# Performance work log

Measured on AMD Instinct MI355X. Metric: run time of the kernel, lower is better.

The kernel has to match this reference:

```python
import jax, jax.numpy as jnp
import numpy as np

BZ, N, NH, HD = 256, 360, 4, 8  # batch, roi_num, num_heads, head_dim
POOL_L = int(N * 0.7)  # 252


def _lrelu(x):
    return jax.nn.leaky_relu(x, 0.2)


def _bn(x, g, b):
    # training-mode BatchNorm1d over flattened (bz*roi) dim, biased variance, eps=1e-5
    mu = x.mean(0)
    var = x.var(0)
    return (x - mu) * jax.lax.rsqrt(var + 1e-5) * g + b


def setup_inputs() -> dict:
    key = jax.random.key(0)
    ks = jax.random.split(key, 20)
    def rn(i, shape, s=0.05):
        return jax.random.normal(ks[i], shape, dtype=jnp.float32) * s
    z = lambda *s: jnp.zeros(s, jnp.float32)
    o = lambda *s: jnp.ones(s, jnp.float32)
    return {
        "m": jax.random.normal(ks[0], (BZ, N, N), dtype=jnp.float32),
        "node_feature": jax.random.normal(ks[1], (BZ, N, N), dtype=jnp.float32),
        "cls": rn(2, (1, 16)),
        "gcn0_w": rn(3, (N, N)), "gcn0_b": z(N),
        "gcn1_w": rn(4, (N, N)), "gcn1_b": z(N),
        "gcn2_w1": rn(5, (N, 64)), "gcn2_b1": z(64),
        "gcn2_w2": rn(6, (64, 16)), "gcn2_b2": z(16),
        "sc_w": rn(7, (N, 16)), "sc_b": z(16),
        "bn0_g": o(N), "bn0_b": z(N),
        "bn1_g": o(N), "bn1_b": z(N),
        "bn2_g": o(16), "bn2_b": z(16),
        "wq": rn(8, (16, NH * HD)), "bq": z(NH * HD),
        "wk": rn(9, (16, NH * HD)), "bk": z(NH * HD),
        "wv": rn(10, (16, NH * HD)), "bv": z(NH * HD),
        "wo": rn(11, (NH * HD, 16)), "bo": z(16),
        "f1_w": rn(12, (16, 64)), "f1_b": z(64),
        "f2_w": rn(13, (64, 32)), "f2_b": z(32),
        "f3_w": rn(14, (32, 2)), "f3_b": z(2),
    }


def reference(m, node_feature, cls, gcn0_w, gcn0_b, gcn1_w, gcn1_b,
              gcn2_w1, gcn2_b1, gcn2_w2, gcn2_b2, sc_w, sc_b,
              bn0_g, bn0_b, bn1_g, bn1_b, bn2_g, bn2_b,
              wq, bq, wk, bk, wv, bv, wo, bo,
              f1_w, f1_b, f2_w, f2_b, f3_w, f3_b):
    bz, n = m.shape[0], m.shape[1]
    # einsum('ijk,ijp->ijp', m, x) == rowsum(m) * x (elementwise), faithful to source
    rowsum = m.sum(-1, keepdims=True)  # [bz, n, 1]

    x_clone = jnp.zeros_like(node_feature)
    x = node_feature
    # layer 0
    x = rowsum * x
    x = _lrelu(x @ gcn0_w + gcn0_b) + x_clone
    x = _bn(x.reshape(bz * n, -1), bn0_g, bn0_b).reshape(bz, n, -1)
    x_clone = x
    # layer 1
    x = rowsum * x
    x = _lrelu(x @ gcn1_w + gcn1_b) + x_clone
    x = _bn(x.reshape(bz * n, -1), bn1_g, bn1_b).reshape(bz, n, -1)
    x_clone = x
    # layer 2 (with shortcut projection)
    x = rowsum * x
    h = _lrelu(_lrelu(x @ gcn2_w1 + gcn2_b1) @ gcn2_w2 + gcn2_b2)
    x = h + _lrelu(x_clone @ sc_w + sc_b)
    x = _bn(x.reshape(bz * n, -1), bn2_g, bn2_b).reshape(bz, n, 16)

    # prepend cls token (vectorized, replaces the per-sample python loop)
    x_in = jnp.concatenate([jnp.broadcast_to(cls, (bz, 1, 16)), x], axis=1)  # [bz, n+1, 16]

    # Encoder: multi-head self-attention
    q = (x_in @ wq + bq).reshape(bz, n + 1, NH, HD)
    k = (x_in @ wk + bk).reshape(bz, n + 1, NH, HD)
    v = (x_in @ wv + bv).reshape(bz, n + 1, NH, HD)
    scale = 1.0 / jnp.sqrt(jnp.asarray(HD, jnp.float32))
    attn = jax.nn.softmax(jnp.einsum('bqhd,bkhd->bhqk', q, k) * scale, axis=-1)  # [bz,4,n+1,n+1]
    out = jnp.einsum('bhqk,bkhd->bqhd', attn, v).reshape(bz, n + 1, NH * HD) @ wo + bo  # [bz,n+1,16]

    # cls-row attention summed over 4 heads, drop cls column
    score = attn[:, :, 0, :].sum(1)[:, 1:]  # [bz, n]
    sc = score
    vals, idx = jax.lax.top_k(score, POOL_L)  # top-l sort/gather
    w = jax.nn.softmax(vals, axis=-1)  # [bz, l]
    x_body = out[:, 1:, :]  # [bz, n, 16]
    x_p = jnp.take_along_axis(x_body, idx[:, :, None], axis=1)  # [bz, l, 16]
    pooled = jnp.einsum('bl,bld->bd', w, x_p)  # [bz, 16]

    h = _lrelu(pooled @ f1_w + f1_b)
    h = _lrelu(h @ f2_w + f2_b)
    logits = h @ f3_w + f3_b  # [bz, 2]
    return (logits, jax.nn.sigmoid(sc), attn)
```

## Files before the change

kernel.cpp:

```cpp
#include <hip/hip_runtime.h>
#include <math.h>

#define BZ 256
#define NN 360
#define NP1 361
#define MROWS (BZ*NN)
#define POOLL 252
#define KP 384

typedef __attribute__((ext_vector_type(8))) short bf16x8;
typedef __attribute__((ext_vector_type(4))) float f32x4;

__device__ __forceinline__ float lrelu(float x){ return x > 0.f ? x : 0.2f*x; }

__device__ __forceinline__ ushort f2bf(float f){
    union { float f; uint u; } v; v.f = f;
    uint u = v.u + 0x7FFFu + ((v.u >> 16) & 1u);
    return (ushort)(u >> 16);
}
__device__ __forceinline__ float bf2f(ushort h){
    union { uint u; float f; } v; v.u = ((uint)h) << 16;
    return v.f;
}
__device__ __forceinline__ void split2(float v, ushort& hi, ushort& lo){
    hi = f2bf(v);
    lo = f2bf(v - bf2f(hi));
}

__device__ __forceinline__ void gload16(const void* g, void* l){
    __builtin_amdgcn_global_load_lds((const __attribute__((address_space(1))) uint*)g,
                                     (__attribute__((address_space(3))) uint*)l, 16, 0, 0);
}

__device__ __forceinline__ void stage_plane(const ushort* __restrict__ src, size_t srow0,
                                            ushort (*P)[32], int k0, int t){
    int w = t >> 6;
    #pragma unroll
    for (int i=0;i<2;i++){
        int u = i*256 + t;
        int row = u >> 2, ccs = u & 3;
        int cg = ccs ^ ((row >> 1) & 3);
        const ushort* g = src + (srow0 + row)*KP + k0 + cg*8;
        char* l = (char*)P + i*4096 + w*1024;
        gload16(g, l);
    }
}

__device__ __forceinline__ bf16x8 frag_read(const ushort (*P)[32], int row, int g){
    return *(const bf16x8*)((const char*)P + row*64 + ((g ^ ((row >> 1) & 3)) * 16));
}

__global__ void k_zero(float* p, int n){
    int i = blockIdx.x*blockDim.x + threadIdx.x;
    if (i < n) p[i] = 0.f;
}

__global__ __launch_bounds__(256)
void k_rowsum(const float* __restrict__ m, float* __restrict__ rowsum){
    int wid = (blockIdx.x*blockDim.x + threadIdx.x) >> 6;
    int lane = threadIdx.x & 63;
    if (wid >= MROWS) return;
    const float4* p = (const float4*)(m + (size_t)wid*NN);
    float s = 0.f;
    {
        float4 f = p[lane];
        s += f.x + f.y + f.z + f.w;
    }
    if (lane < 26){
        float4 f = p[64 + lane];
        s += f.x + f.y + f.z + f.w;
    }
    #pragma unroll
    for (int off = 32; off; off >>= 1) s += __shfl_down(s, off);
    if (lane == 0) rowsum[wid] = s;
}

__global__ __launch_bounds__(384)
void k_prepw(const float* __restrict__ W, int ncols, int joff,
             const float* __restrict__ s, const float* __restrict__ h,
             ushort* __restrict__ Wth, ushort* __restrict__ Wtl, float* __restrict__ cvec)
{
    int j = blockIdx.x;
    int k = threadIdx.x;
    __shared__ float red[6];
    float wv = 0.f, hv = 0.f, sv = 1.f;
    if (k < NN && j < ncols){
        wv = W[(size_t)k*ncols + j];
        if (s) sv = s[k];
        if (h) hv = h[k];
    }
    ushort hi, lo; split2(wv * sv, hi, lo);
    Wth[(size_t)(joff + j)*KP + k] = hi;
    Wtl[(size_t)(joff + j)*KP + k] = lo;
    float v = hv * wv;
    #pragma unroll
    for (int off = 32; off; off >>= 1) v += __shfl_down(v, off);
    int lane = k & 63, wid = k >> 6;
    if (lane == 0) red[wid] = v;
    __syncthreads();
    if (k == 0) cvec[joff + j] = red[0]+red[1]+red[2]+red[3]+red[4]+red[5];
}

template<bool AF32, bool RESID>
__global__ __launch_bounds__(256)
void k_gemm_mfma(const void* __restrict__ Avh, const ushort* __restrict__ Avl,
                 const ushort* __restrict__ Wth, const ushort* __restrict__ Wtl,
                 const float* __restrict__ cvec, const float* __restrict__ bias,
                 const float* __restrict__ rowsum,
                 const float* __restrict__ bns, const float* __restrict__ bnh,
                 ushort* __restrict__ Yhi, ushort* __restrict__ Ylo,
                 float* __restrict__ colsum, float* __restrict__ colsq)
{
    __shared__ ushort Ah[128][32];
    __shared__ ushort Al[128][32];
    __shared__ ushort Bh[128][32];
    __shared__ ushort Bl[128][32];
    int t = threadIdx.x;
    int w = t >> 6, lane = t & 63;
    int l15 = lane & 15, g = lane >> 4;
    int idx = blockIdx.x;
    int gr = idx & 7;
    int rem = idx >> 3;
    int jcb = rem % 3;
    int gq = rem / 3;
    int rowblk = (gq*8 + gr) * 128;
    int colblk = jcb * 128;

    f32x4 acc[2][8];
    #pragma unroll
    for (int i=0;i<2;i++)
        #pragma unroll
        for (int j=0;j<8;j++)
            #pragma unroll
            for (int e=0;e<4;e++) acc[i][j][e] = 0.f;

    for (int kt = 0; kt < 12; ++kt){
        int k0 = kt * 32;
        if (AF32){
            const float* A = (const float*)Avh;
            int row = t >> 1, half = t & 1;
            int fr = (row >> 1) & 3;
            #pragma unroll
            for (int c=0;c<2;c++){
                int cg = half*2 + c;
                int k = k0 + cg*8;
                float4 f0 = make_float4(0.f,0.f,0.f,0.f);
                float4 f1 = make_float4(0.f,0.f,0.f,0.f);
                if (k < NN){
                    f0 = *(const float4*)&A[(size_t)(rowblk+row)*NN + k];
                    f1 = *(const float4*)&A[(size_t)(rowblk+row)*NN + k + 4];
                }
                ushort h0,l0,h1,l1,h2,l2,h3,l3,h4,l4,h5,l5,h6,l6,h7,l7;
                split2(f0.x,h0,l0); split2(f0.y,h1,l1); split2(f0.z,h2,l2); split2(f0.w,h3,l3);
                split2(f1.x,h4,l4); split2(f1.y,h5,l5); split2(f1.z,h6,l6); split2(f1.w,h7,l7);
                uint4 hv = make_uint4((uint)h0|((uint)h1<<16), (uint)h2|((uint)h3<<16),
                                      (uint)h4|((uint)h5<<16), (uint)h6|((uint)h7<<16));
                uint4 lv = make_uint4((uint)l0|((uint)l1<<16), (uint)l2|((uint)l3<<16),
                                      (uint)l4|((uint)l5<<16), (uint)l6|((uint)l7<<16));
                int ccs = cg ^ fr;
                *(uint4*)((char*)Ah + row*64 + ccs*16) = hv;
                *(uint4*)((char*)Al + row*64 + ccs*16) = lv;
            }
        } else {
            stage_plane((const ushort*)Avh, (size_t)rowblk, Ah, k0, t);
            stage_plane(Avl,               (size_t)rowblk, Al, k0, t);
        }
        stage_plane(Wth, (size_t)colblk, Bh, k0, t);
        stage_plane(Wtl, (size_t)colblk, Bl, k0, t);
        __syncthreads();

        bf16x8 ah0 = frag_read(Ah, 32*w + l15, g);
        bf16x8 ah1 = frag_read(Ah, 32*w + 16 + l15, g);
        bf16x8 al0 = frag_read(Al, 32*w + l15, g);
        bf16x8 al1 = frag_read(Al, 32*w + 16 + l15, g);
        #pragma unroll
        for (int nj=0;nj<8;nj++){
            bf16x8 bh = frag_read(Bh, 16*nj + l15, g);
            bf16x8 bl = frag_read(Bl, 16*nj + l15, g);
            acc[0][nj] = __builtin_amdgcn_mfma_f32_16x16x32_bf16(ah0, bh, acc[0][nj], 0, 0, 0);
            acc[0][nj] = __builtin_amdgcn_mfma_f32_16x16x32_bf16(al0, bh, acc[0][nj], 0, 0, 0);
            acc[0][nj] = __builtin_amdgcn_mfma_f32_16x16x32_bf16(ah0, bl, acc[0][nj], 0, 0, 0);
            acc[1][nj] = __builtin_amdgcn_mfma_f32_16x16x32_bf16(ah1, bh, acc[1][nj], 0, 0, 0);
            acc[1][nj] = __builtin_amdgcn_mfma_f32_16x16x32_bf16(al1, bh, acc[1][nj], 0, 0, 0);
            acc[1][nj] = __builtin_amdgcn_mfma_f32_16x16x32_bf16(ah1, bl, acc[1][nj], 0, 0, 0);
        }
        __syncthreads();
    }

    const ushort* AHg = (const ushort*)Avh;
    float cs_part[8] = {0,0,0,0,0,0,0,0}, cq_part[8] = {0,0,0,0,0,0,0,0};
    #pragma unroll
    for (int mi=0;mi<2;mi++){
        #pragma unroll
        for (int nj=0;nj<8;nj++){
            f32x4 d = acc[mi][nj];
            #pragma unroll
            for (int r=0;r<4;r++){
                int row = rowblk + 32*w + 16*mi + 4*g + r;
                int col = colblk + 16*nj + l15;
                float v = 0.f;
                if (col < NN){
                    float pre = rowsum[row] * (d[r] + cvec[col]) + bias[col];
                    v = lrelu(pre);
                    if (RESID){
                        size_t ai = (size_t)row*KP + col;
                        float ar = bf2f(AHg[ai]) + bf2f(Avl[ai]);
                        v += ar * bns[col] + bnh[col];
                    }
                }
                ushort hi, lo; split2(v, hi, lo);
                Yhi[(size_t)row*KP + col] = hi;
                Ylo[(size_t)row*KP + col] = lo;
                cs_part[nj] += v;
                cq_part[nj] += v*v;
            }
        }
    }
    #pragma unroll
    for (int nj=0;nj<8;nj++){
        cs_part[nj] += __shfl_xor(cs_part[nj], 16); cs_part[nj] += __shfl_xor(cs_part[nj], 32);
        cq_part[nj] += __shfl_xor(cq_part[nj], 16); cq_part[nj] += __shfl_xor(cq_part[nj], 32);
    }
    float* red = (float*)&Ah[0][0];
    if (lane < 16){
        #pragma unroll
        for (int nj=0;nj<8;nj++) red[w*128 + nj*16 + l15] = cs_part[nj];
    }
    __syncthreads();
    if (t < 128 && colblk + t < NN)
        atomicAdd(&colsum[colblk + t], red[t] + red[128+t] + red[256+t] + red[384+t]);
    __syncthreads();
    if (lane < 16){
        #pragma unroll
        for (int nj=0;nj<8;nj++) red[w*128 + nj*16 + l15] = cq_part[nj];
    }
    __syncthreads();
    if (t < 128 && colblk + t < NN)
        atomicAdd(&colsq[colblk + t], red[t] + red[128+t] + red[256+t] + red[384+t]);
}

__global__ void k_bnfin(const float* __restrict__ colsum, const float* __restrict__ colsq,
                        const float* __restrict__ g, const float* __restrict__ b, int ncols,
                        float* __restrict__ scale, float* __restrict__ shift){
    int j = blockIdx.x*blockDim.x + threadIdx.x;
    if (j >= ncols) return;
    float mu = colsum[j] / (float)MROWS;
    float var = colsq[j] / (float)MROWS - mu*mu;
    float sc = g[j] * rsqrtf(var + 1e-5f);
    scale[j] = sc;
    shift[j] = b[j] - mu*sc;
}

__global__ __launch_bounds__(256)
void k_gemm2_mfma(const ushort* __restrict__ AH, const ushort* __restrict__ AL,
                  const ushort* __restrict__ Wth, const ushort* __restrict__ Wtl,
                  const float* __restrict__ cvec, const float* __restrict__ b1,
                  const float* __restrict__ scb, const float* __restrict__ rowsum,
                  float* __restrict__ h1buf, float* __restrict__ scbuf)
{
    __shared__ ushort Ah[128][32];
    __shared__ ushort Al[128][32];
    __shared__ ushort Bh[80][40];
    __shared__ ushort Bl[80][40];
    int t = threadIdx.x;
    int w = t >> 6, lane = t & 63;
    int l15 = lane & 15, g = lane >> 4;
    int rowblk = blockIdx.x * 128;

    f32x4 acc[2][5];
    #pragma unroll
    for (int i=0;i<2;i++)
        #pragma unroll
        for (int j=0;j<5;j++)
            #pragma unroll
            for (int e=0;e<4;e++) acc[i][j][e] = 0.f;

    for (int kt = 0; kt < 12; ++kt){
        int k0 = kt * 32;
        stage_plane(AH, (size_t)rowblk, Ah, k0, t);
        stage_plane(AL, (size_t)rowblk, Al, k0, t);
        #pragma unroll
        for (int l=0;l<2;l++){
            int c = t + l*256;
            if (c < 320){
                int col = c >> 2, kk = (c & 3)*8;
                ((int4*)&Bh[col][kk])[0] = *(const int4*)&Wth[(size_t)col*KP + k0 + kk];
                ((int4*)&Bl[col][kk])[0] = *(const int4*)&Wtl[(size_t)col*KP + k0 + kk];
            }
        }
        __syncthreads();
        bf16x8 ah0 = frag_read(Ah, 32*w + l15, g);
        bf16x8 ah1 = frag_read(Ah, 32*w + 16 + l15, g);
        bf16x8 al0 = frag_read(Al, 32*w + l15, g);
        bf16x8 al1 = frag_read(Al, 32*w + 16 + l15, g);
        #pragma unroll
        for (int nj=0;nj<5;nj++){
            bf16x8 bh = *(const bf16x8*)&Bh[16*nj + l15][8*g];
            bf16x8 bl = *(const bf16x8*)&Bl[16*nj + l15][8*g];
            acc[0][nj] = __builtin_amdgcn_mfma_f32_16x16x32_bf16(ah0, bh, acc[0][nj], 0, 0, 0);
            acc[0][nj] = __builtin_amdgcn_mfma_f32_16x16x32_bf16(al0, bh, acc[0][nj], 0, 0, 0);
            acc[0][nj] = __builtin_amdgcn_mfma_f32_16x16x32_bf16(ah0, bl, acc[0][nj], 0, 0, 0);
            acc[1][nj] = __builtin_amdgcn_mfma_f32_16x16x32_bf16(ah1, bh, acc[1][nj], 0, 0, 0);
            acc[1][nj] = __builtin_amdgcn_mfma_f32_16x16x32_bf16(al1, bh, acc[1][nj], 0, 0, 0);
            acc[1][nj] = __builtin_amdgcn_mfma_f32_16x16x32_bf16(ah1, bl, acc[1][nj], 0, 0, 0);
        }
        __syncthreads();
    }

    #pragma unroll
    for (int mi=0;mi<2;mi++){
        #pragma unroll
        for (int nj=0;nj<5;nj++){
            f32x4 d = acc[mi][nj];
            #pragma unroll
            for (int r=0;r<4;r++){
                int row = rowblk + 32*w + 16*mi + 4*g + r;
                int col = 16*nj + l15;
                if (nj < 4){
                    float pre = rowsum[row] * (d[r] + cvec[col]) + b1[col];
                    h1buf[(size_t)row*64 + col] = lrelu(pre);
                } else {
                    int cc = col - 64;
                    float pre = d[r] + cvec[col] + scb[cc];
                    scbuf[(size_t)row*16 + cc] = lrelu(pre);
                }
            }
        }
    }
}

__global__ __launch_bounds__(256)
void k_stage2(const float* __restrict__ h1buf, const float* __restrict__ scbuf,
              const float* __restrict__ w2, const float* __restrict__ b2,
              float* __restrict__ x2, float* __restrict__ colsum, float* __restrict__ colsq)
{
    __shared__ float Hs[64][65];
    __shared__ float Ws[64][17];
    __shared__ float red[16][16];
    int t = threadIdx.x;
    int rowblk = blockIdx.x * 64;
    #pragma unroll
    for (int l=0;l<4;l++){
        int idx = t + l*256;
        Ws[idx>>4][idx&15] = w2[idx];
    }
    #pragma unroll
    for (int l=0;l<16;l++){
        int idx = t + l*256;
        Hs[idx>>6][idx&63] = h1buf[(size_t)rowblk*64 + idx];
    }
    __syncthreads();
    int col = t & 15, rb = t >> 4;
    float ps=0.f, pq=0.f;
    #pragma unroll
    for (int gg=0; gg<4; gg++){
        int r = rb + gg*16;
        float s = b2[col];
        #pragma unroll
        for (int c=0;c<64;c++) s += Hs[r][c]*Ws[c][col];
        float v = lrelu(s) + scbuf[(size_t)(rowblk+r)*16 + col];
        x2[(size_t)(rowblk+r)*16 + col] = v;
        ps += v; pq += v*v;
    }
    red[rb][col] = ps; __syncthreads();
    if (t < 16){
        float s=0.f;
        for (int g=0; g<16; g++) s += red[g][t];
        atomicAdd(&colsum[t], s);
    }
    __syncthreads();
    red[rb][col] = pq; __syncthreads();
    if (t < 16){
        float s=0.f;
        for (int g=0; g<16; g++) s += red[g][t];
        atomicAdd(&colsq[t], s);
    }
}

__global__ __launch_bounds__(256)
void k_qkv(const float* __restrict__ x2, const float* __restrict__ s2, const float* __restrict__ h2,
           const float* __restrict__ cls,
           const float* __restrict__ wq, const float* __restrict__ bq,
           const float* __restrict__ wk, const float* __restrict__ bk,
           const float* __restrict__ wv, const float* __restrict__ bv,
           float* __restrict__ qkv)
{
    int b = blockIdx.x;
    __shared__ float4 xin[NP1][4];
    int t = threadIdx.x;
    for (int i = t; i < NP1*4; i += 256){
        int r = i >> 2, c4 = i & 3;
        float4 f;
        if (r == 0) f = ((const float4*)cls)[c4];
        else {
            f = *(const float4*)&x2[((size_t)b*NN + r-1)*16 + c4*4];
            f.x = f.x*s2[c4*4+0] + h2[c4*4+0];
            f.y = f.y*s2[c4*4+1] + h2[c4*4+1];
            f.z = f.z*s2[c4*4+2] + h2[c4*4+2];
            f.w = f.w*s2[c4*4+3] + h2[c4*4+3];
        }
        xin[r][c4] = f;
    }
    __syncthreads();
    for (int task = t; task < 3*NP1*8; task += 256){
        int tn = task / (NP1*8);
        int rem = task - tn*(NP1*8);
        int r = rem >> 3, d4 = rem & 7;
        const float* W  = (tn==0) ? wq : ((tn==1) ? wk : wv);
        const float* Bb = (tn==0) ? bq : ((tn==1) ? bk : bv);
        float o0 = Bb[d4*4+0], o1 = Bb[d4*4+1], o2 = Bb[d4*4+2], o3 = Bb[d4*4+3];
        #pragma unroll
        for (int c4=0;c4<4;c4++){
            float4 xf = xin[r][c4];
            float xs[4] = {xf.x, xf.y, xf.z, xf.w};
            #pragma unroll
            for (int cc=0;cc<4;cc++){
                int c = c4*4 + cc;
                float x = xs[cc];
                o0 += x * W[c*32 + d4*4 + 0];
                o1 += x * W[c*32 + d4*4 + 1];
                o2 += x * W[c*32 + d4*4 + 2];
                o3 += x * W[c*32 + d4*4 + 3];
            }
        }
        if (tn == 0){
            const float sc = 0.35355339059327373f;
            o0 *= sc; o1 *= sc; o2 *= sc; o3 *= sc;
        }
        *(float4*)&qkv[(((size_t)b*3 + tn)*NP1 + r)*32 + d4*4] = make_float4(o0,o1,o2,o3);
    }
}

__device__ __forceinline__ float bfly8(float o[8], int lane){
    int b0 = lane & 1, b1 = lane & 2, b2 = lane & 4;
    float n[4];
    #pragma unroll
    for (int j=0;j<4;j++){
        float give = b0 ? o[j] : o[j+4];
        float keep = b0 ? o[j+4] : o[j];
        n[j] = keep + __shfl_xor(give, 1);
    }
    float m2[2];
    #pragma unroll
    for (int j=0;j<2;j++){
        float give = b1 ? n[j] : n[j+2];
        float keep = b1 ? n[j+2] : n[j];
        m2[j] = keep + __shfl_xor(give, 2);
    }
    float give = b2 ? m2[0] : m2[1];
    float keep = b2 ? m2[1] : m2[0];
    float v = keep + __shfl_xor(give, 4);
    v += __shfl_xor(v, 8);
    v += __shfl_xor(v, 16);
    v += __shfl_xor(v, 32);
    return v;
}

__global__ __launch_bounds__(256)
void k_attn(const float* __restrict__ qkv, float* __restrict__ attn, float* __restrict__ obuf)
{
    int blk = blockIdx.x;
    int chunk = blk & 1;
    int bh = blk >> 1;
    int b = bh >> 2, h = bh & 3;
    __shared__ float4 KV[4][NP1];
    __shared__ float4 QS[2][NP1];
    int t = threadIdx.x;

    const float* qb = qkv + ((size_t)b*3 + 0)*NP1*32 + h*8;
    const float* kb = qkv + ((size_t)b*3 + 1)*NP1*32 + h*8;
    const float* vb = qkv + ((size_t)b*3 + 2)*NP1*32 + h*8;
    for (int i = t; i < NP1*6; i += 256){
        int r = i / 6, s = i - 6*(i/6);
        int dq = s & 1;
        if (s < 2)      QS[dq][r]   = *(const float4*)&qb[(size_t)r*32 + dq*4];
        else if (s < 4) KV[dq][r]   = *(const float4*)&kb[(size_t)r*32 + dq*4];
        else            KV[2+dq][r] = *(const float4*)&vb[(size_t)r*32 + dq*4];
    }
    __syncthreads();

    int w = t >> 6, lane = t & 63;
    float kreg[6][8], vreg[6][8];
    #pragma unroll
    for (int j=0;j<6;j++){
        int ki = lane + (j<<6);
        int kc = ki > 360 ? 360 : ki;
        float4 ka = KV[0][kc], kb2 = KV[1][kc];
        float4 va = KV[2][kc], vb2 = KV[3][kc];
        kreg[j][0]=ka.x; kreg[j][1]=ka.y; kreg[j][2]=ka.z; kreg[j][3]=ka.w;
        kreg[j][4]=kb2.x; kreg[j][5]=kb2.y; kreg[j][6]=kb2.z; kreg[j][7]=kb2.w;
        vreg[j][0]=va.x; vreg[j][1]=va.y; vreg[j][2]=va.z; vreg[j][3]=va.w;
        vreg[j][4]=vb2.x; vreg[j][5]=vb2.y; vreg[j][6]=vb2.z; vreg[j][7]=vb2.w;
    }

    int cbase = chunk * 181;
    int cend  = chunk ? NP1 : 181;

    for (int qi0 = cbase + (w<<1); qi0 < cend; qi0 += 8){
        int qi1 = qi0 + 1;
        bool v1 = (qi1 < cend);

        float q0[8], q1[8];
        {
            float4 a = QS[0][qi0], c = QS[1][qi0];
            q0[0]=a.x;q0[1]=a.y;q0[2]=a.z;q0[3]=a.w;q0[4]=c.x;q0[5]=c.y;q0[6]=c.z;q0[7]=c.w;
            float4 a1 = QS[0][qi1], c1 = QS[1][qi1];
            q1[0]=a1.x;q1[1]=a1.y;q1[2]=a1.z;q1[3]=a1.w;q1[4]=c1.x;q1[5]=c1.y;q1[6]=c1.z;q1[7]=c1.w;
        }

        float e0[6], e1[6];
        float mx0 = -1e30f, mx1 = -1e30f;
        #pragma unroll
        for (int j=0;j<6;j++){
            int ki = lane + (j<<6);
            float s0 = 0.f, s1 = 0.f;
            #pragma unroll
            for (int d=0;d<8;d++){ s0 += q0[d]*kreg[j][d]; s1 += q1[d]*kreg[j][d]; }
            if (ki >= NP1){ s0 = -1e30f; s1 = -1e30f; }
            e0[j] = s0; e1[j] = s1;
            mx0 = fmaxf(mx0, s0); mx1 = fmaxf(mx1, s1);
        }
        #pragma unroll
        for (int off=32; off; off>>=1){
            mx0 = fmaxf(mx0, __shfl_xor(mx0, off));
            mx1 = fmaxf(mx1, __shfl_xor(mx1, off));
        }
        float sum0 = 0.f, sum1 = 0.f;
        #pragma unroll
        for (int j=0;j<6;j++){
            float p0 = __expf(e0[j]-mx0);
            float p1 = __expf(e1[j]-mx1);
            e0[j]=p0; e1[j]=p1;
            sum0 += p0; sum1 += p1;
        }
        #pragma unroll
        for (int off=32; off; off>>=1){
            sum0 += __shfl_xor(sum0, off);
            sum1 += __shfl_xor(sum1, off);
        }
        float inv0 = 1.f/sum0;
        float inv1 = 1.f/sum1;

        size_t abase = (size_t)bh*NP1*NP1 + (size_t)qi0*NP1;
        float o0[8] = {0,0,0,0,0,0,0,0};
        float o1[8] = {0,0,0,0,0,0,0,0};
        #pragma unroll
        for (int j=0;j<6;j++){
            int ki = lane + (j<<6);
            float p0 = e0[j]*inv0;
            float p1 = e1[j]*inv1;
            if (ki < NP1){
                attn[abase + ki] = p0;
                if (v1) attn[abase + NP1 + ki] = p1;
            }
            #pragma unroll
            for (int d=0;d<8;d++){
                o0[d] += p0*vreg[j][d];
                o1[d] += p1*vreg[j][d];
            }
        }
        float val0 = bfly8(o0, lane);
        float val1 = bfly8(o1, lane);
        int l7 = lane & 7;
        int dmap = ((l7&1)<<2) | (l7&2) | ((l7>>2)&1);
        if (lane < 8)
            obuf[((size_t)b*NP1 + qi0)*32 + h*8 + dmap] = val0;
        else if (lane < 16 && v1)
            obuf[((size_t)b*NP1 + qi1)*32 + h*8 + dmap] = val1;
    }
}

__global__ __launch_bounds__(256)
void k_pool(const float* __restrict__ attn, const float* __restrict__ obuf,
            const float* __restrict__ wo, const float* __restrict__ bo,
            const float* __restrict__ f1w, const float* __restrict__ f1b,
            const float* __restrict__ f2w, const float* __restrict__ f2b,
            const float* __restrict__ f3w, const float* __restrict__ f3b,
            float* __restrict__ out_sig, float* __restrict__ logits)
{
    int b = blockIdx.x;
    __shared__ float sc[NN];
    __shared__ float w[NN];
    __shared__ float red[256];
    __shared__ float pooled32[32];
    __shared__ float p16[16];
    __shared__ float h64[64];
    __shared__ float h32[32];
    int t = threadIdx.x;
    for (int i=t; i<NN; i+=256){
        float s = 0.f;
        #pragma unroll
        for (int h=0; h<4; h++)
            s += attn[(((size_t)b*4+h)*NP1)*NP1 + 1 + i];
        sc[i] = s;
        out_sig[b*NN + i] = 1.f/(1.f + __expf(-s));
    }
    __syncthreads();
    float mx = -1e30f;
    for (int i=t; i<NN; i+=256) mx = fmaxf(mx, sc[i]);
    red[t] = mx; __syncthreads();
    for (int s=128; s; s>>=1){ if (t<s) red[t]=fmaxf(red[t],red[t+s]); __syncthreads(); }
    mx = red[0];
    __syncthreads();
    float psum = 0.f;
    for (int i=t; i<NN; i+=256){
        float si = sc[i];
        int r = 0;
        for (int j=0;j<NN;j++){
            float sj = sc[j];
            r += (sj > si) || (sj == si && j < i);
        }
        float wi = (r < POOLL) ? __expf(si - mx) : 0.f;
        w[i] = wi;
        psum += wi;
    }
    red[t] = psum; __syncthreads();
    for (int s=128; s; s>>=1){ if (t<s) red[t]+=red[t+s]; __syncthreads(); }
    float inv = 1.f / red[0];
    __syncthreads();
    if (t < 32){
        float s = 0.f;
        for (int i=0;i<NN;i++) s += w[i] * obuf[((size_t)b*NP1 + 1 + i)*32 + t];
        pooled32[t] = s * inv;
    }
    __syncthreads();
    if (t < 16){
        float s = bo[t];
        for (int d=0;d<32;d++) s += pooled32[d]*wo[d*16+t];
        p16[t] = s;
    }
    __syncthreads();
    if (t < 64){
        float s = f1b[t];
        for (int c=0;c<16;c++) s += p16[c]*f1w[c*64+t];
        h64[t] = lrelu(s);
    }
    __syncthreads();
    if (t < 32){
        float s = f2b[t];
        for (int c=0;c<64;c++) s += h64[c]*f2w[c*32+t];
        h32[t] = lrelu(s);
    }
    __syncthreads();
    if (t < 2){
        float s = f3b[t];
        for (int c=0;c<32;c++) s += h32[c]*f3w[c*2+t];
        logits[b*2+t] = s;
    }
}

extern "C" void kernel_launch(void* const* d_in, const int* in_sizes, int n_in,
                              void* d_out, int out_size, void* d_ws, size_t ws_size,
                              hipStream_t stream)
{
    const float* m    = (const float*)d_in[0];
    const float* nf   = (const float*)d_in[1];
    const float* cls  = (const float*)d_in[2];
    const float* g0w  = (const float*)d_in[3];
    const float* g0b  = (const float*)d_in[4];
    const float* g1w  = (const float*)d_in[5];
    const float* g1b  = (const float*)d_in[6];
    const float* g2w1 = (const float*)d_in[7];
    const float* g2b1 = (const float*)d_in[8];
    const float* g2w2 = (const float*)d_in[9];
    const float* g2b2 = (const float*)d_in[10];
    const float* scw  = (const float*)d_in[11];
    const float* scb  = (const float*)d_in[12];
    const float* bn0g = (const float*)d_in[13];
    const float* bn0b = (const float*)d_in[14];
    const float* bn1g = (const float*)d_in[15];
    const float* bn1b = (const float*)d_in[16];
    const float* bn2g = (const float*)d_in[17];
    const float* bn2b = (const float*)d_in[18];
    const float* wq = (const float*)d_in[19];
    const float* bq = (const float*)d_in[20];
    const float* wk = (const float*)d_in[21];
    const float* bk = (const float*)d_in[22];
    const float* wv = (const float*)d_in[23];
    const float* bv = (const float*)d_in[24];
    const float* wo = (const float*)d_in[25];
    const float* bo = (const float*)d_in[26];
    const float* f1w = (const float*)d_in[27];
    const float* f1b = (const float*)d_in[28];
    const float* f2w = (const float*)d_in[29];
    const float* f2b = (const float*)d_in[30];
    const float* f3w = (const float*)d_in[31];
    const float* f3b = (const float*)d_in[32];

    float* out_logits = (float*)d_out;
    float* out_sig = out_logits + 512;
    float* attn = out_sig + (size_t)BZ*NN;

    char* base = (char*)attn;
    const size_t szy = (size_t)MROWS * KP * 2;
    ushort* y0h = (ushort*)base;
    ushort* y0l = (ushort*)(base + szy);
    ushort* y1h = (ushort*)(base + 2*szy);
    ushort* y1l = (ushort*)(base + 3*szy);
    float*  h1buf = (float*)(base + 4*szy);
    const size_t szh = (size_t)MROWS * 64 * 4;
    float*  scbuf = (float*)(base + 4*szy + szh);
    const size_t szsc = (size_t)MROWS * 16 * 4;
    ushort* Wt0h = (ushort*)(base + 4*szy + szh + szsc);
    ushort* Wt0l = Wt0h + (size_t)KP*KP;
    ushort* Wt1h = Wt0l + (size_t)KP*KP;
    ushort* Wt1l = Wt1h + (size_t)KP*KP;
    ushort* Wt2h = Wt1l + (size_t)KP*KP;
    ushort* Wt2l = Wt2h + (size_t)KP*KP;
    float*  c0  = (float*)(Wt2l + (size_t)KP*KP);
    float*  c1  = c0 + KP;
    float*  c2  = c1 + KP;

    float* ws = (float*)d_ws;
    float* rowsum = ws;                ws += MROWS;
    float* stats  = ws;                ws += 1472;
    float* cs0 = stats, *cq0 = stats+360, *cs1 = stats+720, *cq1 = stats+1080,
         * cs2 = stats+1440, *cq2 = stats+1456;
    float* s0 = ws;  ws += 360;
    float* h0 = ws;  ws += 360;
    float* s1 = ws;  ws += 360;
    float* hh1 = ws; ws += 360;
    float* s2 = ws;  ws += 16;
    float* h2 = ws;  ws += 16;
    float* x2 = ws;       ws += (size_t)MROWS*16;
    float* obuf = ws;     ws += (size_t)BZ*NP1*32;
    float* qkv = ws;      ws += (size_t)BZ*3*NP1*32;

    k_zero<<<6, 256, 0, stream>>>(stats, 1472);
    k_rowsum<<<MROWS/4, 256, 0, stream>>>(m, rowsum);
    k_prepw<<<KP, KP, 0, stream>>>(g0w, 360, 0, nullptr, nullptr, Wt0h, Wt0l, c0);

    k_gemm_mfma<true,false><<<2160, 256, 0, stream>>>(nf, nullptr, Wt0h, Wt0l, c0, g0b, rowsum, nullptr, nullptr, y0h, y0l, cs0, cq0);
    k_bnfin<<<1, 384, 0, stream>>>(cs0, cq0, bn0g, bn0b, 360, s0, h0);
    k_prepw<<<KP, KP, 0, stream>>>(g1w, 360, 0, s0, h0, Wt1h, Wt1l, c1);
    k_gemm_mfma<false,true><<<2160, 256, 0, stream>>>(y0h, y0l, Wt1h, Wt1l, c1, g1b, rowsum, s0, h0, y1h, y1l, cs1, cq1);
    k_bnfin<<<1, 384, 0, stream>>>(cs1, cq1, bn1g, bn1b, 360, s1, hh1);
    k_prepw<<<64, KP, 0, stream>>>(g2w1, 64, 0, s1, hh1, Wt2h, Wt2l, c2);
    k_prepw<<<16, KP, 0, stream>>>(scw, 16, 64, s1, hh1, Wt2h, Wt2l, c2);
    k_gemm2_mfma<<<720, 256, 0, stream>>>(y1h, y1l, Wt2h, Wt2l, c2, g2b1, scb, rowsum, h1buf, scbuf);
    k_stage2<<<1440, 256, 0, stream>>>(h1buf, scbuf, g2w2, g2b2, x2, cs2, cq2);
    k_bnfin<<<1, 64, 0, stream>>>(cs2, cq2, bn2g, bn2b, 16, s2, h2);
    k_qkv<<<BZ, 256, 0, stream>>>(x2, s2, h2, cls, wq, bq, wk, bk, wv, bv, qkv);
    k_attn<<<BZ*4*2, 256, 0, stream>>>(qkv, attn, obuf);
    k_pool<<<BZ, 256, 0, stream>>>(attn, obuf, wo, bo, f1w, f1b, f2w, f2b, f3w, f3b, out_sig, out_logits);
}
```

Before: 742.0 us.

## Fuse second GCN stage into gemm2 epilogue, merge zeroing, drop Q staging

Fuses the small 64->16 stage-2 MLP and its BN statistics into the gemm2 MFMA kernel's epilogue, reusing shared memory for the hidden activations. This removes the h1buf/scbuf round trip through global memory and one kernel launch. It also folds the stats zeroing into the rowsum kernel, and makes the attention kernel read Q directly from global memory instead of staging it in LDS. The trade-off is more shared memory per block in the fused kernel, which may cut occupancy, plus extra global loads for Q in the attention loop.

```diff
diff --git a/kernel.cpp b/kernel.cpp
--- a/kernel.cpp
+++ b/kernel.cpp
@@ -50,14 +50,11 @@
     return *(const bf16x8*)((const char*)P + row*64 + ((g ^ ((row >> 1) & 3)) * 16));
 }
 
-__global__ void k_zero(float* p, int n){
-    int i = blockIdx.x*blockDim.x + threadIdx.x;
-    if (i < n) p[i] = 0.f;
-}
-
 __global__ __launch_bounds__(256)
-void k_rowsum(const float* __restrict__ m, float* __restrict__ rowsum){
-    int wid = (blockIdx.x*blockDim.x + threadIdx.x) >> 6;
+void k_rowsum(const float* __restrict__ m, float* __restrict__ rowsum, float* __restrict__ stats){
+    int gi = blockIdx.x*blockDim.x + threadIdx.x;
+    if (gi < 1472) stats[gi] = 0.f;
+    int wid = gi >> 6;
     int lane = threadIdx.x & 63;
     if (wid >= MROWS) return;
     const float4* p = (const float4*)(m + (size_t)wid*NN);
@@ -252,16 +249,19 @@
 }
 
 __global__ __launch_bounds__(256)
-void k_gemm2_mfma(const ushort* __restrict__ AH, const ushort* __restrict__ AL,
-                  const ushort* __restrict__ Wth, const ushort* __restrict__ Wtl,
-                  const float* __restrict__ cvec, const float* __restrict__ b1,
-                  const float* __restrict__ scb, const float* __restrict__ rowsum,
-                  float* __restrict__ h1buf, float* __restrict__ scbuf)
+void k_gemm2_fused(const ushort* __restrict__ AH, const ushort* __restrict__ AL,
+                   const ushort* __restrict__ Wth, const ushort* __restrict__ Wtl,
+                   const float* __restrict__ cvec, const float* __restrict__ b1,
+                   const float* __restrict__ scb, const float* __restrict__ rowsum,
+                   const float* __restrict__ w2, const float* __restrict__ b2,
+                   float* __restrict__ x2, float* __restrict__ colsum, float* __restrict__ colsq)
 {
-    __shared__ ushort Ah[128][32];
-    __shared__ ushort Al[128][32];
-    __shared__ ushort Bh[80][40];
-    __shared__ ushort Bl[80][40];
+    __shared__ __align__(16) char smem[46848];
+    ushort (*Ah)[32] = (ushort(*)[32])smem;
+    ushort (*Al)[32] = (ushort(*)[32])(smem + 8192);
+    ushort (*Bh)[40] = (ushort(*)[40])(smem + 16384);
+    ushort (*Bl)[40] = (ushort(*)[40])(smem + 16384 + 6400);
+
     int t = threadIdx.x;
     int w = t >> 6, lane = t & 63;
     int l15 = lane & 15, g = lane >> 4;
@@ -307,6 +307,9 @@
         __syncthreads();
     }
 
+    float (*Hs)[65] = (float(*)[65])smem;
+    float (*Sc)[16] = (float(*)[16])(smem + 33280);
+    float (*Ws)[17] = (float(*)[17])(smem + 41472);
     #pragma unroll
     for (int mi=0;mi<2;mi++){
         #pragma unroll
@@ -314,65 +317,50 @@
             f32x4 d = acc[mi][nj];
             #pragma unroll
             for (int r=0;r<4;r++){
-                int row = rowblk + 32*w + 16*mi + 4*g + r;
+                int lrow = 32*w + 16*mi + 4*g + r;
+                int row = rowblk + lrow;
                 int col = 16*nj + l15;
                 if (nj < 4){
                     float pre = rowsum[row] * (d[r] + cvec[col]) + b1[col];
-                    h1buf[(size_t)row*64 + col] = lrelu(pre);
+                    Hs[lrow][col] = lrelu(pre);
                 } else {
-                    int cc = col - 64;
-                    float pre = d[r] + cvec[col] + scb[cc];
-                    scbuf[(size_t)row*16 + cc] = lrelu(pre);
+                    Sc[lrow][col-64] = lrelu(d[r] + cvec[col] + scb[col-64]);
                 }
             }
         }
     }
-}
-
-__global__ __launch_bounds__(256)
-void k_stage2(const float* __restrict__ h1buf, const float* __restrict__ scbuf,
-              const float* __restrict__ w2, const float* __restrict__ b2,
-              float* __restrict__ x2, float* __restrict__ colsum, float* __restrict__ colsq)
-{
-    __shared__ float Hs[64][65];
-    __shared__ float Ws[64][17];
-    __shared__ float red[16][16];
-    int t = threadIdx.x;
-    int rowblk = blockIdx.x * 64;
     #pragma unroll
     for (int l=0;l<4;l++){
-        int idx = t + l*256;
-        Ws[idx>>4][idx&15] = w2[idx];
-    }
-    #pragma unroll
-    for (int l=0;l<16;l++){
-        int idx = t + l*256;
-        Hs[idx>>6][idx&63] = h1buf[(size_t)rowblk*64 + idx];
-    }
-    __syncthreads();
+        int i2 = t + l*256;
+        Ws[i2>>4][i2&15] = w2[i2];
+    }
+    __syncthreads();
+
     int col = t & 15, rb = t >> 4;
-    float ps=0.f, pq=0.f;
-    #pragma unroll
-    for (int gg=0; gg<4; gg++){
+    float ps = 0.f, pq = 0.f;
+    #pragma unroll
+    for (int gg=0; gg<8; gg++){
         int r = rb + gg*16;
         float s = b2[col];
         #pragma unroll
         for (int c=0;c<64;c++) s += Hs[r][c]*Ws[c][col];
-        float v = lrelu(s) + scbuf[(size_t)(rowblk+r)*16 + col];
+        float v = lrelu(s) + Sc[r][col];
         x2[(size_t)(rowblk+r)*16 + col] = v;
         ps += v; pq += v*v;
     }
+    __syncthreads();
+    float (*red)[16] = (float(*)[16])smem;
     red[rb][col] = ps; __syncthreads();
     if (t < 16){
-        float s=0.f;
-        for (int g=0; g<16; g++) s += red[g][t];
+        float s = 0.f;
+        for (int g2=0; g2<16; g2++) s += red[g2][t];
         atomicAdd(&colsum[t], s);
     }
     __syncthreads();
     red[rb][col] = pq; __syncthreads();
     if (t < 16){
-        float s=0.f;
-        for (int g=0; g<16; g++) s += red[g][t];
+        float s = 0.f;
+        for (int g2=0; g2<16; g2++) s += red[g2][t];
         atomicAdd(&colsq[t], s);
     }
 }
@@ -464,18 +452,16 @@
     int bh = blk >> 1;
     int b = bh >> 2, h = bh & 3;
     __shared__ float4 KV[4][NP1];
-    __shared__ float4 QS[2][NP1];
     int t = threadIdx.x;
 
     const float* qb = qkv + ((size_t)b*3 + 0)*NP1*32 + h*8;
     const float* kb = qkv + ((size_t)b*3 + 1)*NP1*32 + h*8;
     const float* vb = qkv + ((size_t)b*3 + 2)*NP1*32 + h*8;
-    for (int i = t; i < NP1*6; i += 256){
-        int r = i / 6, s = i - 6*(i/6);
+    for (int i = t; i < NP1*4; i += 256){
+        int r = i >> 2, s = i & 3;
         int dq = s & 1;
-        if (s < 2)      QS[dq][r]   = *(const float4*)&qb[(size_t)r*32 + dq*4];
-        else if (s < 4) KV[dq][r]   = *(const float4*)&kb[(size_t)r*32 + dq*4];
-        else            KV[2+dq][r] = *(const float4*)&vb[(size_t)r*32 + dq*4];
+        const float* src = (s < 2) ? kb : vb;
+        KV[(s < 2 ? 0 : 2) + dq][r] = *(const float4*)&src[(size_t)r*32 + dq*4];
     }
     __syncthreads();
 
@@ -499,12 +485,15 @@
     for (int qi0 = cbase + (w<<1); qi0 < cend; qi0 += 8){
         int qi1 = qi0 + 1;
         bool v1 = (qi1 < cend);
+        int q1r = v1 ? qi1 : qi0;
 
         float q0[8], q1[8];
         {
-            float4 a = QS[0][qi0], c = QS[1][qi0];
+            float4 a  = *(const float4*)&qb[(size_t)qi0*32];
+            float4 c  = *(const float4*)&qb[(size_t)qi0*32 + 4];
+            float4 a1 = *(const float4*)&qb[(size_t)q1r*32];
+            float4 c1 = *(const float4*)&qb[(size_t)q1r*32 + 4];
             q0[0]=a.x;q0[1]=a.y;q0[2]=a.z;q0[3]=a.w;q0[4]=c.x;q0[5]=c.y;q0[6]=c.z;q0[7]=c.w;
-            float4 a1 = QS[0][qi1], c1 = QS[1][qi1];
             q1[0]=a1.x;q1[1]=a1.y;q1[2]=a1.z;q1[3]=a1.w;q1[4]=c1.x;q1[5]=c1.y;q1[6]=c1.z;q1[7]=c1.w;
         }
 
@@ -697,11 +686,7 @@
     ushort* y0l = (ushort*)(base + szy);
     ushort* y1h = (ushort*)(base + 2*szy);
     ushort* y1l = (ushort*)(base + 3*szy);
-    float*  h1buf = (float*)(base + 4*szy);
-    const size_t szh = (size_t)MROWS * 64 * 4;
-    float*  scbuf = (float*)(base + 4*szy + szh);
-    const size_t szsc = (size_t)MROWS * 16 * 4;
-    ushort* Wt0h = (ushort*)(base + 4*szy + szh + szsc);
+    ushort* Wt0h = (ushort*)(base + 4*szy);
     ushort* Wt0l = Wt0h + (size_t)KP*KP;
     ushort* Wt1h = Wt0l + (size_t)KP*KP;
     ushort* Wt1l = Wt1h + (size_t)KP*KP;
@@ -726,8 +711,7 @@
     float* obuf = ws;     ws += (size_t)BZ*NP1*32;
     float* qkv = ws;      ws += (size_t)BZ*3*NP1*32;
 
-    k_zero<<<6, 256, 0, stream>>>(stats, 1472);
-    k_rowsum<<<MROWS/4, 256, 0, stream>>>(m, rowsum);
+    k_rowsum<<<MROWS/4, 256, 0, stream>>>(m, rowsum, stats);
     k_prepw<<<KP, KP, 0, stream>>>(g0w, 360, 0, nullptr, nullptr, Wt0h, Wt0l, c0);
 
     k_gemm_mfma<true,false><<<2160, 256, 0, stream>>>(nf, nullptr, Wt0h, Wt0l, c0, g0b, rowsum, nullptr, nullptr, y0h, y0l, cs0, cq0);
@@ -737,8 +721,7 @@
     k_bnfin<<<1, 384, 0, stream>>>(cs1, cq1, bn1g, bn1b, 360, s1, hh1);
     k_prepw<<<64, KP, 0, stream>>>(g2w1, 64, 0, s1, hh1, Wt2h, Wt2l, c2);
     k_prepw<<<16, KP, 0, stream>>>(scw, 16, 64, s1, hh1, Wt2h, Wt2l, c2);
-    k_gemm2_mfma<<<720, 256, 0, stream>>>(y1h, y1l, Wt2h, Wt2l, c2, g2b1, scb, rowsum, h1buf, scbuf);
-    k_stage2<<<1440, 256, 0, stream>>>(h1buf, scbuf, g2w2, g2b2, x2, cs2, cq2);
+    k_gemm2_fused<<<720, 256, 0, stream>>>(y1h, y1l, Wt2h, Wt2l, c2, g2b1, scb, rowsum, g2w2, g2b2, x2, cs2, cq2);
     k_bnfin<<<1, 64, 0, stream>>>(cs2, cq2, bn2g, bn2b, 16, s2, h2);
     k_qkv<<<BZ, 256, 0, stream>>>(x2, s2, h2, cls, wq, bq, wk, bk, wv, bv, qkv);
     k_attn<<<BZ*4*2, 256, 0, stream>>>(qkv, attn, obuf);
```

Result: slower. 792.4 us (+6.8%).
